# Kernel tuning notes

Measured on AMD Instinct MI355X. Metric: run time of the kernel, lower is better.

The kernel has to match this reference:

```python
import jax, jax.numpy as jnp
import numpy as np

DIM = 48
HEADS = 4
HIDDEN = DIM * 2  # ffn_expansion_factor=2
EPS = 1e-5


def conv3d(x, w, b, groups=1, pad=0):
    # x: [B,C,T,H,W], w: [O, I//groups, kd,kh,kw]
    y = jax.lax.conv_general_dilated(
        x, w, window_strides=(1, 1, 1), padding=[(pad, pad)] * 3,
        dimension_numbers=('NCDHW', 'OIDHW', 'NCDHW'),
        feature_group_count=groups)
    return y + b[None, :, None, None, None]


def layernorm(x, w, b):
    # WithBias LayerNorm over channel dim (dim=1), per spatial position
    mu = jnp.mean(x, axis=1, keepdims=True)
    var = jnp.var(x, axis=1, keepdims=True)
    return (x - mu) / jnp.sqrt(var + EPS) * w[None, :, None, None, None] + b[None, :, None, None, None]


def setup_inputs() -> dict:
    key = jax.random.key(0)
    ks = jax.random.split(key, 16)
    s = 0.02
    inp = {
        'x': jax.random.normal(ks[0], (2, DIM, 16, 64, 64), jnp.float32),
        'ln1_w': jnp.ones((DIM,), jnp.float32),
        'ln1_b': jnp.zeros((DIM,), jnp.float32),
        'qkv_w': jax.random.normal(ks[1], (DIM * 3 * HEADS, DIM, 1, 1, 1), jnp.float32) * s,
        'qkv_b': jnp.zeros((DIM * 3 * HEADS,), jnp.float32),
        'qkvdw_w': jax.random.normal(ks[2], (DIM * 3 * HEADS, HEADS, 3, 3, 3), jnp.float32) * s,
        'qkvdw_b': jnp.zeros((DIM * 3 * HEADS,), jnp.float32),
        'temperature': jnp.ones((HEADS, 1, 1), jnp.float32),
        'proj_w': jax.random.normal(ks[3], (DIM, DIM * HEADS, 1, 1, 1), jnp.float32) * s,
        'proj_b': jnp.zeros((DIM,), jnp.float32),
        'ln2_w': jnp.ones((DIM,), jnp.float32),
        'ln2_b': jnp.zeros((DIM,), jnp.float32),
        'pin_w': jax.random.normal(ks[4], (2 * HIDDEN, DIM, 1, 1, 1), jnp.float32) * s,
        'pin_b': jnp.zeros((2 * HIDDEN,), jnp.float32),
        'dw_w': jax.random.normal(ks[5], (2 * HIDDEN, 1, 3, 3, 3), jnp.float32) * s,
        'dw_b': jnp.zeros((2 * HIDDEN,), jnp.float32),
        'pout_w': jax.random.normal(ks[6], (DIM, HIDDEN, 1, 1, 1), jnp.float32) * s,
        'pout_b': jnp.zeros((DIM,), jnp.float32),
    }
    return inp


def attention(y, qkv_w, qkv_b, qkvdw_w, qkvdw_b, temperature, proj_w, proj_b):
    b, c, t, h, w = y.shape
    n = t * h * w
    qkv = conv3d(y, qkv_w, qkv_b, pad=0)
    qkv = conv3d(qkv, qkvdw_w, qkvdw_b, groups=c * 3, pad=1)  # groups=dim*3
    q, k, v = jnp.split(qkv, 3, axis=1)  # each [b, heads*dim, t,h,w]
    def resh(z):
        return z.reshape(b, HEADS, c, n)  # 'b (head c) t h w -> b head c (thw)'
    q, k, v = resh(q), resh(k), resh(v)
    q = q / jnp.maximum(jnp.linalg.norm(q, axis=-1, keepdims=True), 1e-12)
    k = k / jnp.maximum(jnp.linalg.norm(k, axis=-1, keepdims=True), 1e-12)
    attn = jnp.einsum('bhcn,bhdn->bhcd', q, k) * temperature[None]  # [b,h,c,c]
    attn = jax.nn.softmax(attn, axis=-1)
    out = jnp.einsum('bhcd,bhdn->bhcn', attn, v)
    out = out.reshape(b, HEADS * c, t, h, w)
    return conv3d(out, proj_w, proj_b, pad=0)


def ffn(y, pin_w, pin_b, dw_w, dw_b, pout_w, pout_b):
    z = conv3d(y, pin_w, pin_b, pad=0)
    z = conv3d(z, dw_w, dw_b, groups=2 * HIDDEN, pad=1)
    z1, z2 = jnp.split(z, 2, axis=1)
    z = jax.nn.gelu(z1, approximate=False) * z2
    return conv3d(z, pout_w, pout_b, pad=0)


def reference(x, ln1_w, ln1_b, qkv_w, qkv_b, qkvdw_w, qkvdw_b, temperature,
              proj_w, proj_b, ln2_w, ln2_b, pin_w, pin_b, dw_w, dw_b, pout_w, pout_b):
    x = x + attention(layernorm(x, ln1_w, ln1_b), qkv_w, qkv_b, qkvdw_w, qkvdw_b,
                      temperature, proj_w, proj_b)
    x = x + ffn(layernorm(x, ln2_w, ln2_b), pin_w, pin_b, dw_w, dw_b, pout_w, pout_b)
    return x
```

## Files before the change

kernel.cpp:

```cpp
#include <hip/hip_runtime.h>
#include <hip/hip_bf16.h>
#include <hip/hip_fp16.h>
#include <hip/hip_fp8.h>
#include <math.h>

typedef __hip_bfloat16 bf16;
typedef __attribute__((ext_vector_type(8))) short short8;
typedef __attribute__((ext_vector_type(4))) float f32x4;

#define NPB   65536
#define DIMC  48
#define C2    192
#define HIDC  96
#define TT    16

static __device__ __forceinline__ float b2f(bf16 v) { return __bfloat162float(v); }
static __device__ __forceinline__ bf16  f2b(float v) { return __float2bfloat16(v); }
static __device__ __forceinline__ float bfr2f(unsigned short u) {
  union { unsigned int i; float f; } c; c.i = ((unsigned int)u) << 16; return c.f;
}
static __device__ __forceinline__ unsigned short f2us(float v) {
  return __bfloat16_as_ushort(__float2bfloat16(v));
}
static __device__ __forceinline__ unsigned char f2fp8(float v) {
  __hip_fp8_e4m3 t(v); return (unsigned char)t.__x;
}
static __device__ __forceinline__ float fp82f(unsigned char u) {
  __hip_fp8_e4m3 t; t.__x = (__hip_fp8_storage_t)u; return (float)t;
}

#if defined(__has_builtin)
#if __has_builtin(__builtin_amdgcn_cvt_pk_f32_fp8) && __has_builtin(__builtin_amdgcn_cvt_pk_fp8_f32)
#define HW_FP8 1
#endif
#endif

static __device__ __forceinline__ void fp8x4_to_f32x4(unsigned int u, float* o) {
#ifdef HW_FP8
  auto lo = __builtin_amdgcn_cvt_pk_f32_fp8(u, false);
  auto hi = __builtin_amdgcn_cvt_pk_f32_fp8(u, true);
  o[0] = lo[0]; o[1] = lo[1]; o[2] = hi[0]; o[3] = hi[1];
#else
  o[0] = fp82f(u & 0xff); o[1] = fp82f((u >> 8) & 0xff);
  o[2] = fp82f((u >> 16) & 0xff); o[3] = fp82f((u >> 24) & 0xff);
#endif
}
static __device__ __forceinline__ unsigned int f32x2_to_fp8pair(float x, float y) {
#ifdef HW_FP8
  return (unsigned int)__builtin_amdgcn_cvt_pk_fp8_f32(x, y, 0, false) & 0xffffu;
#else
  return (unsigned int)f2fp8(x) | ((unsigned int)f2fp8(y) << 8);
#endif
}
static __device__ __forceinline__ void fp8pair_to_2f(unsigned int pr, float& x, float& y) {
#ifdef HW_FP8
  auto d = __builtin_amdgcn_cvt_pk_f32_fp8(pr, false);
  x = d[0]; y = d[1];
#else
  x = fp82f(pr & 0xff); y = fp82f((pr >> 8) & 0xff);
#endif
}

static __device__ __forceinline__ unsigned int pkh2(float x, float y) {
  auto h = __builtin_amdgcn_cvt_pkrtz(x, y);
  return __builtin_bit_cast(unsigned int, h);
}
static __device__ __forceinline__ float dot2f16(unsigned int a, unsigned int b, float c) {
  asm("v_dot2_f32_f16 %0, %1, %2, %0" : "+v"(c) : "v"(a), "v"(b));
  return c;
}
static __device__ __forceinline__ __half2 u2h2(unsigned int u) {
  return __builtin_bit_cast(__half2, u);
}

__global__ __launch_bounds__(256) void k_ln(
    const float* __restrict__ x, const float* __restrict__ lw, const float* __restrict__ lb,
    bf16* __restrict__ y) {
  int p = blockIdx.x * 256 + threadIdx.x;
  int b = p >> 16, n = p & (NPB - 1);
  const float* xb = x + ((size_t)b * DIMC) * NPB + n;
  float v[DIMC]; float s = 0.f, s2 = 0.f;
#pragma unroll
  for (int c = 0; c < DIMC; ++c) { float t = xb[(size_t)c * NPB]; v[c] = t; s += t; s2 += t * t; }
  float mu = s * (1.f / DIMC);
  float var = fmaxf(s2 * (1.f / DIMC) - mu * mu, 0.f);
  float rs = rsqrtf(var + 1e-5f);
  bf16* yb = y + ((size_t)b * DIMC) * NPB + n;
#pragma unroll
  for (int c = 0; c < DIMC; ++c) yb[(size_t)c * NPB] = f2b((v[c] - mu) * rs * lw[c] + lb[c]);
}

__global__ __launch_bounds__(256) void k_pconv_sec(
    const bf16* __restrict__ y, const float* __restrict__ W,
    const float* __restrict__ bias, int hp, unsigned char* __restrict__ dst, int dcs) {
  __shared__ unsigned short Yl[64][130];
  __shared__ unsigned short Wl[48][72];
  __shared__ unsigned char Ot[48][132];
  int tid = threadIdx.x;
  int sec = blockIdx.x;
  int row = (hp >= 0) ? ((sec >> 1) * 192 + (2 * hp + (sec & 1)) * 48) : sec * 48;
  int bt = blockIdx.y;
  int b = bt >> 9;
  int n0 = (bt & 511) * 128;
  const unsigned short* yb = (const unsigned short*)(y + ((size_t)b * DIMC) * NPB) + n0;
  for (int j = tid; j < 48 * 32; j += 256) {
    int c = j >> 5, sub = j & 31;
    ushort4 u = *(const ushort4*)(yb + (size_t)c * NPB + sub * 4);
    *(ushort2*)&Yl[c][sub * 4]     = make_ushort2(u.x, u.y);
    *(ushort2*)&Yl[c][sub * 4 + 2] = make_ushort2(u.z, u.w);
  }
  for (int j = tid; j < 16 * 32; j += 256) {
    int c = 48 + (j >> 5), sub = j & 31;
    *(ushort2*)&Yl[c][sub * 4]     = make_ushort2(0, 0);
    *(ushort2*)&Yl[c][sub * 4 + 2] = make_ushort2(0, 0);
  }
  if (tid < 48) {
    const float* wr = W + (size_t)(row + tid) * 48;
    unsigned short* wl = Wl[tid];
#pragma unroll
    for (int c = 0; c < 48; ++c) wl[c] = f2us(wr[c]);
#pragma unroll
    for (int c = 48; c < 64; ++c) wl[c] = 0;
  }
  __syncthreads();
  int wv = tid >> 6, ln = tid & 63, lq = ln >> 4, li = ln & 15;
  short8 afr[3][2];
#pragma unroll
  for (int mt = 0; mt < 3; ++mt)
#pragma unroll
    for (int ks = 0; ks < 2; ++ks)
      afr[mt][ks] = *(const short8*)&Wl[mt * 16 + li][ks * 32 + lq * 8];
#pragma unroll 1
  for (int ns = 0; ns < 2; ++ns) {
    int nn = wv * 32 + ns * 16 + li;
    short8 bfr[2];
#pragma unroll
    for (int ks = 0; ks < 2; ++ks)
#pragma unroll
      for (int j = 0; j < 8; ++j)
        bfr[ks][j] = (short)Yl[ks * 32 + lq * 8 + j][nn];
#pragma unroll
    for (int mt = 0; mt < 3; ++mt) {
      f32x4 acc = {0.f, 0.f, 0.f, 0.f};
      acc = __builtin_amdgcn_mfma_f32_16x16x32_bf16(afr[mt][0], bfr[0], acc, 0, 0, 0);
      acc = __builtin_amdgcn_mfma_f32_16x16x32_bf16(afr[mt][1], bfr[1], acc, 0, 0, 0);
      int m0 = mt * 16 + lq * 4;
      unsigned int p01 = f32x2_to_fp8pair(16.f * (acc[0] + bias[row + m0]),
                                          16.f * (acc[1] + bias[row + m0 + 1]));
      unsigned int p23 = f32x2_to_fp8pair(16.f * (acc[2] + bias[row + m0 + 2]),
                                          16.f * (acc[3] + bias[row + m0 + 3]));
      Ot[m0 + 0][nn] = (unsigned char)p01;
      Ot[m0 + 1][nn] = (unsigned char)(p01 >> 8);
      Ot[m0 + 2][nn] = (unsigned char)p23;
      Ot[m0 + 3][nn] = (unsigned char)(p23 >> 8);
    }
  }
  __syncthreads();
  for (int j = tid; j < 48 * 32; j += 256) {
    int m = j >> 5, c4 = (j & 31) * 4;
    *(uchar4*)(dst + ((size_t)b * dcs + sec * 48 + m) * NPB + n0 + c4) =
        *(const uchar4*)&Ot[m][c4];
  }
}

__global__ __launch_bounds__(512, 8) void k_gconv48(
    const unsigned char* __restrict__ src, int sco,
    const float* __restrict__ gw, const float* __restrict__ gb,
    unsigned char* __restrict__ dst, int hp, int isV, float* __restrict__ sqout) {
  __shared__ unsigned int tile[2][4][18][66];
  __shared__ unsigned int Wh[2][28][4];
  __shared__ float red[8][4];
  int tid = threadIdx.x;
  int t0 = (blockIdx.x >> 2) * 2, h0 = (blockIdx.x & 3) * 16;
  int cbase = blockIdx.y * 4, b = blockIdx.z;
  int seg = cbase / 48, lc = cbase - seg * 48;
  int wbase = isV ? 384 + (2 * hp + seg) * 48 + lc
                  : ((seg >= 2 ? 192 : 0) + (2 * hp + (seg & 1)) * 48 + lc);
  int dch = isV ? (2 * hp + seg) * 48 + lc : cbase;
  const unsigned char* ib = src + ((size_t)b * 288 + sco + cbase) * NPB;
  for (int j = tid; j < 216; j += 512) {
    int o = j & 3, t2 = j >> 2;
    int cp = t2 / 27, tap = t2 - cp * 27;
    const float* wr = gw + (size_t)(wbase + o) * 108 + cp * 54 + tap;
    Wh[cp][tap][o] = pkh2(wr[0], wr[27]);
  }
  for (int j = tid; j < 2304; j += 512) {
    int sub = j & 15, r = j >> 4;
    int cp = r / 72, rem = r - cp * 72;
    int tt = rem / 18, hh = rem - tt * 18;
    int gt = t0 + tt - 1, gh2 = h0 + hh - 1;
    unsigned int* dp = &tile[cp][tt][hh][1 + sub * 4];
    if ((unsigned)gt < 16u && (unsigned)gh2 < 64u) {
      const unsigned char* p0 = ib + (size_t)(2 * cp) * NPB + gt * 4096 + gh2 * 64 + sub * 4;
      unsigned int u0 = *(const unsigned int*)p0;
      unsigned int u1 = *(const unsigned int*)(p0 + NPB);
      float a0[4], a1[4];
      fp8x4_to_f32x4(u0, a0);
      fp8x4_to_f32x4(u1, a1);
      dp[0] = pkh2(a0[0], a1[0]);
      dp[1] = pkh2(a0[1], a1[1]);
      dp[2] = pkh2(a0[2], a1[2]);
      dp[3] = pkh2(a0[3], a1[3]);
    } else { dp[0] = 0; dp[1] = 0; dp[2] = 0; dp[3] = 0; }
  }
  for (int j = tid; j < 288; j += 512) {
    int side = j & 1, r = j >> 1;
    int cp = r / 72, rem = r - cp * 72;
    int tt = rem / 18, hh = rem - tt * 18;
    tile[cp][tt][hh][side ? 65 : 0] = 0;
  }
  __syncthreads();
  int w = tid & 63, hr = tid >> 6;
  float acc[2][2][4];
#pragma unroll
  for (int t = 0; t < 2; ++t)
#pragma unroll
    for (int i = 0; i < 2; ++i)
#pragma unroll
      for (int o = 0; o < 4; ++o) acc[t][i][o] = 0.f;
#pragma unroll 1
  for (int cp = 0; cp < 2; ++cp) {
#pragma unroll 1
    for (int dw = 0; dw < 3; ++dw) {
      int wwl = w + dw;
      unsigned int v[4][4];
#pragma unroll
      for (int tt = 0; tt < 4; ++tt)
#pragma unroll
        for (int r = 0; r < 4; ++r) v[tt][r] = tile[cp][tt][hr * 2 + r][wwl];
#pragma unroll
      for (int dt = 0; dt < 3; ++dt)
#pragma unroll
        for (int dh = 0; dh < 3; ++dh) {
          uint4 wv = *(const uint4*)&Wh[cp][dt * 9 + dh * 3 + dw][0];
#pragma unroll
          for (int t = 0; t < 2; ++t)
#pragma unroll
            for (int i = 0; i < 2; ++i) {
              unsigned int val = v[t + dt][i + dh];
              acc[t][i][0] = dot2f16(val, wv.x, acc[t][i][0]);
              acc[t][i][1] = dot2f16(val, wv.y, acc[t][i][1]);
              acc[t][i][2] = dot2f16(val, wv.z, acc[t][i][2]);
              acc[t][i][3] = dot2f16(val, wv.w, acc[t][i][3]);
            }
        }
    }
  }
  float s[4] = {0.f, 0.f, 0.f, 0.f};
#pragma unroll
  for (int o = 0; o < 4; ++o) {
    float bias16 = 16.f * gb[wbase + o];
    size_t obase = ((size_t)b * 192 + dch + o) * NPB;
#pragma unroll
    for (int t = 0; t < 2; ++t) {
      unsigned int pr = f32x2_to_fp8pair(acc[t][0][o] + bias16, acc[t][1][o] + bias16);
      size_t rb = obase + (t0 + t) * 4096 + (h0 + hr * 2) * 64 + w;
      dst[rb]      = (unsigned char)pr;
      dst[rb + 64] = (unsigned char)(pr >> 8);
      if (sqout) {
        float f0, f1; fp8pair_to_2f(pr, f0, f1);
        s[o] = fmaf(f0, f0, fmaf(f1, f1, s[o]));
      }
    }
  }
  if (sqout) {
#pragma unroll
    for (int o = 0; o < 4; ++o) {
      float sv = s[o];
#pragma unroll
      for (int off = 32; off; off >>= 1) sv += __shfl_down(sv, off);
      if ((tid & 63) == 0) red[tid >> 6][o] = sv;
    }
    __syncthreads();
    if (tid < 4) {
      int sqi = (seg < 2 ? 0 : 384) + b * 192 + (2 * hp + (seg & 1)) * 48 + lc + tid;
      float acc8 = 0.f;
#pragma unroll
      for (int k = 0; k < 8; ++k) acc8 += red[k][tid];
      atomicAdd(&sqout[sqi], acc8);
    }
  }
}

__global__ __launch_bounds__(256) void k_gram_mfma(
    const unsigned char* __restrict__ qkd, int hp, float* __restrict__ Gm) {
  __shared__ unsigned short qkl[2][48][264];
  int tid = threadIdx.x, b = blockIdx.y, z = blockIdx.z;
  int wv = tid >> 6, ln = tid & 63, lq = ln >> 4, li = ln & 15;
  const unsigned char* qb = qkd + ((size_t)b * 192 + z * 48) * NPB + blockIdx.x * 1024;
  const unsigned char* kb = qkd + ((size_t)b * 192 + 96 + z * 48) * NPB + blockIdx.x * 1024;
  f32x4 acc[9];
#pragma unroll
  for (int t = 0; t < 9; ++t) acc[t] = (f32x4){0.f, 0.f, 0.f, 0.f};
#pragma unroll 1
  for (int it = 0; it < 4; ++it) {
    __syncthreads();
    for (int j = tid; j < 48 * 64; j += 256) {
      int c = j >> 6, sub = j & 63;
      unsigned int uq = *(const unsigned int*)(qb + (size_t)c * NPB + it * 256 + sub * 4);
      unsigned int uk = *(const unsigned int*)(kb + (size_t)c * NPB + it * 256 + sub * 4);
      float aq[4], ak[4];
      fp8x4_to_f32x4(uq, aq);
      fp8x4_to_f32x4(uk, ak);
      *(ushort2*)&qkl[0][c][sub * 4]     = make_ushort2(f2us(aq[0]), f2us(aq[1]));
      *(ushort2*)&qkl[0][c][sub * 4 + 2] = make_ushort2(f2us(aq[2]), f2us(aq[3]));
      *(ushort2*)&qkl[1][c][sub * 4]     = make_ushort2(f2us(ak[0]), f2us(ak[1]));
      *(ushort2*)&qkl[1][c][sub * 4 + 2] = make_ushort2(f2us(ak[2]), f2us(ak[3]));
    }
    __syncthreads();
    short8 afr[3][2], bfr[3][2];
#pragma unroll
    for (int ks = 0; ks < 2; ++ks) {
      int kbase = wv * 64 + ks * 32 + lq * 8;
#pragma unroll
      for (int t = 0; t < 3; ++t) {
        afr[t][ks] = *(const short8*)&qkl[0][t * 16 + li][kbase];
        bfr[t][ks] = *(const short8*)&qkl[1][t * 16 + li][kbase];
      }
    }
#pragma unroll
    for (int mt = 0; mt < 3; ++mt)
#pragma unroll
      for (int nt = 0; nt < 3; ++nt) {
        acc[mt * 3 + nt] = __builtin_amdgcn_mfma_f32_16x16x32_bf16(afr[mt][0], bfr[nt][0], acc[mt * 3 + nt], 0, 0, 0);
        acc[mt * 3 + nt] = __builtin_amdgcn_mfma_f32_16x16x32_bf16(afr[mt][1], bfr[nt][1], acc[mt * 3 + nt], 0, 0, 0);
      }
  }
  __syncthreads();
  float* red = (float*)&qkl[0][0][0];
  if (wv > 0) {
    float* rw = red + (size_t)(wv - 1) * 2304;
#pragma unroll
    for (int t = 0; t < 9; ++t)
#pragma unroll
      for (int r = 0; r < 4; ++r)
        rw[t * 256 + r * 64 + ln] = acc[t][r];
  }
  __syncthreads();
  if (wv == 0) {
    int hd = 2 * hp + z;
    float* gbase = Gm + (size_t)(b * 4 + hd) * 2304;
#pragma unroll
    for (int t = 0; t < 9; ++t) {
      int mt = t / 3, nt = t - mt * 3;
#pragma unroll
      for (int r = 0; r < 4; ++r) {
        int o = t * 256 + r * 64 + ln;
        float v = acc[t][r] + red[o] + red[2304 + o] + red[4608 + o];
        atomicAdd(&gbase[(mt * 16 + lq * 4 + r) * 48 + nt * 16 + li], v);
      }
    }
  }
}

__global__ __launch_bounds__(256) void k_attn_mm(
    const float* __restrict__ Gm, const float* __restrict__ sq, const float* __restrict__ temp,
    const float* __restrict__ pw, bf16* __restrict__ Mm) {
  __shared__ float A[48][48];
  __shared__ float nk[48];
  int tid = threadIdx.x;
  int bh = blockIdx.x; int b = bh >> 2, hd = bh & 3;
  if (tid >= 64 && tid < 112)
    nk[tid - 64] = fmaxf(sqrtf(sq[384 + bh * 48 + tid - 64]), 1e-12f);
  __syncthreads();
  if (tid < 48) {
    float tv = temp[hd];
    float rq = 1.f / fmaxf(sqrtf(sq[bh * 48 + tid]), 1e-12f);
    const float* grow = Gm + (size_t)bh * 2304 + tid * 48;
    float mx = -1e30f;
#pragma unroll
    for (int d = 0; d < 48; ++d) mx = fmaxf(mx, grow[d] * rq / nk[d] * tv);
    float sum = 0.f;
#pragma unroll
    for (int d = 0; d < 48; ++d) {
      float e = expf(grow[d] * rq / nk[d] * tv - mx);
      A[tid][d] = e; sum += e;
    }
    float inv = 1.f / sum;
#pragma unroll
    for (int d = 0; d < 48; ++d) A[tid][d] *= inv;
  }
  __syncthreads();
  for (int j = tid; j < 2304; j += 256) {
    int m = j / 48, d = j - m * 48;
    float a = 0.f;
#pragma unroll
    for (int c = 0; c < 48; ++c) a = fmaf(pw[m * 192 + hd * 48 + c], A[c][d], a);
    Mm[((size_t)b * 48 + m) * 192 + hd * 48 + d] = f2b(a * 0.0625f);
  }
}

__global__ __launch_bounds__(256) void k_av192(
    const unsigned char* __restrict__ vd8, const bf16* __restrict__ Mm,
    const float* __restrict__ pb, const float* __restrict__ x, float* __restrict__ outp) {
  __shared__ unsigned short Yl[96][130];
  __shared__ unsigned short Ml[48][200];
  int tid = threadIdx.x;
  int bt = blockIdx.x;
  int b = bt >> 9;
  int n0 = (bt & 511) * 128;
  int wv = tid >> 6, ln = tid & 63, lq = ln >> 4, li = ln & 15;
  const unsigned short* mb = (const unsigned short*)(Mm + (size_t)b * 48 * 192);
  for (int j = tid; j < 48 * 48; j += 256) {
    int m = j / 48, c4 = j - m * 48;
    *(ushort4*)&Ml[m][c4 * 4] = *(const ushort4*)(mb + m * 192 + c4 * 4);
  }
  const unsigned char* vb = vd8 + ((size_t)b * C2) * NPB + n0;
  f32x4 acc[3][2];
#pragma unroll
  for (int mt = 0; mt < 3; ++mt)
#pragma unroll
    for (int ns = 0; ns < 2; ++ns) acc[mt][ns] = (f32x4){0.f, 0.f, 0.f, 0.f};
#pragma unroll 1
  for (int s = 0; s < 2; ++s) {
    __syncthreads();
    for (int j = tid; j < 96 * 32; j += 256) {
      int c = j >> 5, sub = j & 31;
      unsigned int u = *(const unsigned int*)(vb + (size_t)(s * 96 + c) * NPB + sub * 4);
      float a[4]; fp8x4_to_f32x4(u, a);
      *(ushort2*)&Yl[c][sub * 4]     = make_ushort2(f2us(a[0]), f2us(a[1]));
      *(ushort2*)&Yl[c][sub * 4 + 2] = make_ushort2(f2us(a[2]), f2us(a[3]));
    }
    __syncthreads();
#pragma unroll 1
    for (int ns = 0; ns < 2; ++ns) {
      int nn = wv * 32 + ns * 16 + li;
      short8 bfr[3];
#pragma unroll
      for (int ks = 0; ks < 3; ++ks)
#pragma unroll
        for (int j = 0; j < 8; ++j)
          bfr[ks][j] = (short)Yl[ks * 32 + lq * 8 + j][nn];
#pragma unroll
      for (int mt = 0; mt < 3; ++mt) {
        short8 a0 = *(const short8*)&Ml[mt * 16 + li][s * 96 + lq * 8];
        short8 a1 = *(const short8*)&Ml[mt * 16 + li][s * 96 + 32 + lq * 8];
        short8 a2 = *(const short8*)&Ml[mt * 16 + li][s * 96 + 64 + lq * 8];
        acc[mt][ns] = __builtin_amdgcn_mfma_f32_16x16x32_bf16(a0, bfr[0], acc[mt][ns], 0, 0, 0);
        acc[mt][ns] = __builtin_amdgcn_mfma_f32_16x16x32_bf16(a1, bfr[1], acc[mt][ns], 0, 0, 0);
        acc[mt][ns] = __builtin_amdgcn_mfma_f32_16x16x32_bf16(a2, bfr[2], acc[mt][ns], 0, 0, 0);
      }
    }
  }
#pragma unroll
  for (int ns = 0; ns < 2; ++ns) {
    int nn = wv * 32 + ns * 16 + li;
#pragma unroll
    for (int mt = 0; mt < 3; ++mt)
#pragma unroll
      for (int r = 0; r < 4; ++r) {
        int m = mt * 16 + lq * 4 + r;
        size_t idx = ((size_t)b * DIMC + m) * NPB + n0 + nn;
        outp[idx] = x[idx] + pb[m] + acc[mt][ns][r];
      }
  }
}

__global__ __launch_bounds__(256) void k_ek96(
    const unsigned char* __restrict__ V, const float* __restrict__ W, int wrs,
    const float* __restrict__ bias, const float* __restrict__ addend, float* __restrict__ outp) {
  __shared__ unsigned short Yl[96][130];
  __shared__ unsigned short Wl[48][104];
  int tid = threadIdx.x;
  int bt = blockIdx.x;
  int b = bt >> 9;
  int n0 = (bt & 511) * 128;
  const unsigned char* vb = V + ((size_t)b * 96) * NPB + n0;
  for (int j = tid; j < 96 * 32; j += 256) {
    int c = j >> 5, sub = j & 31;
    unsigned int u = *(const unsigned int*)(vb + (size_t)c * NPB + sub * 4);
    float a[4]; fp8x4_to_f32x4(u, a);
    *(ushort2*)&Yl[c][sub * 4]     = make_ushort2(f2us(a[0]), f2us(a[1]));
    *(ushort2*)&Yl[c][sub * 4 + 2] = make_ushort2(f2us(a[2]), f2us(a[3]));
  }
  if (tid < 48) {
    const float* wr = W + (size_t)tid * wrs;
    unsigned short* wl = Wl[tid];
#pragma unroll
    for (int c = 0; c < 96; ++c) wl[c] = f2us(wr[c] * 0.0625f);
  }
  __syncthreads();
  int wv = tid >> 6, ln = tid & 63, lq = ln >> 4, li = ln & 15;
  short8 afr[3][3];
#pragma unroll
  for (int mt = 0; mt < 3; ++mt)
#pragma unroll
    for (int ks = 0; ks < 3; ++ks)
      afr[mt][ks] = *(const short8*)&Wl[mt * 16 + li][ks * 32 + lq * 8];
#pragma unroll 1
  for (int ns = 0; ns < 2; ++ns) {
    int nn = wv * 32 + ns * 16 + li;
    short8 bfr[3];
#pragma unroll
    for (int ks = 0; ks < 3; ++ks)
#pragma unroll
      for (int j = 0; j < 8; ++j)
        bfr[ks][j] = (short)Yl[ks * 32 + lq * 8 + j][nn];
#pragma unroll
    for (int mt = 0; mt < 3; ++mt) {
      f32x4 acc = {0.f, 0.f, 0.f, 0.f};
      acc = __builtin_amdgcn_mfma_f32_16x16x32_bf16(afr[mt][0], bfr[0], acc, 0, 0, 0);
      acc = __builtin_amdgcn_mfma_f32_16x16x32_bf16(afr[mt][1], bfr[1], acc, 0, 0, 0);
      acc = __builtin_amdgcn_mfma_f32_16x16x32_bf16(afr[mt][2], bfr[2], acc, 0, 0, 0);
#pragma unroll
      for (int r = 0; r < 4; ++r) {
        int m = mt * 16 + lq * 4 + r;
        size_t idx = ((size_t)b * DIMC + m) * NPB + n0 + nn;
        outp[idx] = acc[r] + addend[idx] + bias[m];
      }
    }
  }
}

__global__ __launch_bounds__(256) void k_dw_gelu(
    const unsigned char* __restrict__ z, const float* __restrict__ dwW,
    const float* __restrict__ dwB, unsigned char* __restrict__ g) {
  __shared__ unsigned int tile[4][18][68];
  int tid = threadIdx.x;
  int t0 = (blockIdx.x >> 2) * 2, h0 = (blockIdx.x & 3) * 16;
  int c = blockIdx.y, b = blockIdx.z;
  int wq = tid & 15, hq = tid >> 4;
  int w0 = wq * 4;
  const unsigned char* zp0 = z + ((size_t)b * C2 + c) * NPB;
  const unsigned char* zp1 = zp0 + (size_t)HIDC * NPB;
  for (int j = tid; j < 72 * 16; j += 256) {
    int r = j >> 4, sub = j & 15;
    int tt = r / 18, hh = r - tt * 18;
    int gt = t0 + tt - 1, gh = h0 + hh - 1;
    unsigned int* dp = &tile[tt][hh][1 + sub * 4];
    if ((unsigned)gt < 16u && (unsigned)gh < 64u) {
      size_t off = (size_t)gt * 4096 + gh * 64 + sub * 4;
      unsigned int u0 = *(const unsigned int*)(zp0 + off);
      unsigned int u1 = *(const unsigned int*)(zp1 + off);
      float a0[4], a1[4];
      fp8x4_to_f32x4(u0, a0);
      fp8x4_to_f32x4(u1, a1);
      dp[0] = pkh2(a0[0], a1[0]);
      dp[1] = pkh2(a0[1], a1[1]);
      dp[2] = pkh2(a0[2], a1[2]);
      dp[3] = pkh2(a0[3], a1[3]);
    } else { dp[0] = 0; dp[1] = 0; dp[2] = 0; dp[3] = 0; }
  }
  for (int j = tid; j < 144; j += 256) {
    int r = j >> 1, side = j & 1;
    int tt = r / 18, hh = r - tt * 18;
    tile[tt][hh][side ? 65 : 0] = 0;
  }
  unsigned int wpk[27];
  {
    const float* wt0 = dwW + (size_t)c * 27;
    const float* wt1 = dwW + (size_t)(c + HIDC) * 27;
#pragma unroll
    for (int tap = 0; tap < 27; ++tap) wpk[tap] = pkh2(wt0[tap], wt1[tap]);
  }
  __syncthreads();
  __half2 hacc[2][4];
#pragma unroll
  for (int t = 0; t < 2; ++t)
#pragma unroll
    for (int k = 0; k < 4; ++k) hacc[t][k] = u2h2(0u);
#pragma unroll 1
  for (int dh = 0; dh < 3; ++dh) {
    unsigned int v[4][6];
#pragma unroll
    for (int tt = 0; tt < 4; ++tt) {
      uint4 q4 = *(const uint4*)&tile[tt][hq + dh][w0];
      uint2 q2 = *(const uint2*)&tile[tt][hq + dh][w0 + 4];
      v[tt][0] = q4.x; v[tt][1] = q4.y; v[tt][2] = q4.z; v[tt][3] = q4.w;
      v[tt][4] = q2.x; v[tt][5] = q2.y;
    }
#pragma unroll
    for (int dt = 0; dt < 3; ++dt)
#pragma unroll
      for (int dw = 0; dw < 3; ++dw) {
        __half2 wk = u2h2(wpk[dt * 9 + dh * 3 + dw]);
#pragma unroll
        for (int t = 0; t < 2; ++t)
#pragma unroll
          for (int k = 0; k < 4; ++k)
            hacc[t][k] = __hfma2(u2h2(v[t + dt][dw + k]), wk, hacc[t][k]);
      }
  }
  float b1 = dwB[c], b2v = dwB[c + HIDC];
  size_t obase = ((size_t)b * HIDC + c) * NPB;
#pragma unroll
  for (int t = 0; t < 2; ++t) {
    float e[4];
#pragma unroll
    for (int k = 0; k < 4; ++k) {
      float x1v = __low2float(hacc[t][k]) * 0.0625f + b1;
      float x2v = __high2float(hacc[t][k]) * 0.0625f + b2v;
      float ge = 0.5f * x1v * (1.f + erff(x1v * 0.70710678118654752f));
      e[k] = 16.f * ge * x2v;
    }
    unsigned int p01 = f32x2_to_fp8pair(e[0], e[1]);
    unsigned int p23 = f32x2_to_fp8pair(e[2], e[3]);
    unsigned int packed = p01 | (p23 << 16);
    *(unsigned int*)(g + obase + (t0 + t) * 4096 + (h0 + hq) * 64 + w0) = packed;
  }
}

extern "C" void kernel_launch(void* const* d_in, const int* in_sizes, int n_in,
                              void* d_out, int out_size, void* d_ws, size_t ws_size,
                              hipStream_t stream) {
  (void)in_sizes; (void)n_in; (void)out_size; (void)ws_size;
  const float* x     = (const float*)d_in[0];
  const float* ln1w  = (const float*)d_in[1];
  const float* ln1b  = (const float*)d_in[2];
  const float* qkvw  = (const float*)d_in[3];
  const float* qkvb  = (const float*)d_in[4];
  const float* gdww  = (const float*)d_in[5];
  const float* gdwb  = (const float*)d_in[6];
  const float* temp  = (const float*)d_in[7];
  const float* projw = (const float*)d_in[8];
  const float* projb = (const float*)d_in[9];
  const float* ln2w  = (const float*)d_in[10];
  const float* ln2b  = (const float*)d_in[11];
  const float* pinw  = (const float*)d_in[12];
  const float* pinb  = (const float*)d_in[13];
  const float* dww   = (const float*)d_in[14];
  const float* dwb   = (const float*)d_in[15];
  const float* poutw = (const float*)d_in[16];
  const float* poutb = (const float*)d_in[17];
  float* out = (float*)d_out;

  char* ws = (char*)d_ws;
  bf16*  y     = (bf16*)(ws);
  unsigned char* st288 = (unsigned char*)(ws + 12582912);
  unsigned char* vd8   = (unsigned char*)(ws + 50331648);
  float* Gm    = (float*)(ws + 75497472);
  float* sq    = (float*)(ws + 75571200);
  bf16*  Mm    = (bf16*)(ws + 75574272);
  unsigned char* qkd8 = (unsigned char*)d_out;
  bf16*  y2    = (bf16*)(ws);
  unsigned char* z8  = (unsigned char*)(ws + 12582912);
  unsigned char* gg8 = (unsigned char*)(ws + 37748736);

  (void)hipMemsetAsync(Gm, 0, 73728 + 3072, stream);
  k_ln<<<dim3(512), dim3(256), 0, stream>>>(x, ln1w, ln1b, y);

  for (int hp = 0; hp < 2; ++hp) {
    k_pconv_sec<<<dim3(6, 1024), dim3(256), 0, stream>>>(y, qkvw, qkvb, hp, st288, 288);
    k_gconv48<<<dim3(32, 48, 2), dim3(512), 0, stream>>>(
        st288, 0, gdww, gdwb, qkd8, hp, 0, sq);
    k_gram_mfma<<<dim3(64, 2, 2), dim3(256), 0, stream>>>(qkd8, hp, Gm);
    k_gconv48<<<dim3(32, 24, 2), dim3(512), 0, stream>>>(
        st288, 192, gdww, gdwb, vd8, hp, 1, nullptr);
  }
  k_attn_mm<<<dim3(8), dim3(256), 0, stream>>>(Gm, sq, temp, projw, Mm);
  k_av192<<<dim3(1024), dim3(256), 0, stream>>>(vd8, Mm, projb, x, out);

  k_ln<<<dim3(512), dim3(256), 0, stream>>>(out, ln2w, ln2b, y2);
  k_pconv_sec<<<dim3(4, 1024), dim3(256), 0, stream>>>(y2, pinw, pinb, -1, z8, 192);
  k_dw_gelu<<<dim3(32, 96, 2), dim3(256), 0, stream>>>(z8, dww, dwb, gg8);
  k_ek96<<<dim3(1024), dim3(256), 0, stream>>>(gg8, poutw, 96, poutb, out, out);
}
```

Before: 522.9 us.

## Rewrite grouped 3x3x3 conv as MFMA with block-diagonal weights

```diff
diff --git a/kernel.cpp b/kernel.cpp
--- a/kernel.cpp
+++ b/kernel.cpp
@@ -72,6 +72,7 @@
 static __device__ __forceinline__ __half2 u2h2(unsigned int u) {
   return __builtin_bit_cast(__half2, u);
 }
+static __device__ __forceinline__ int swz8(int c) { return c ^ ((c >> 4) & 7); }
 
 __global__ __launch_bounds__(256) void k_ln(
     const float* __restrict__ x, const float* __restrict__ lw, const float* __restrict__ lb,
@@ -163,121 +164,129 @@
   }
 }
 
-__global__ __launch_bounds__(512, 8) void k_gconv48(
+__global__ __launch_bounds__(512, 4) void k_gconv48(
     const unsigned char* __restrict__ src, int sco,
     const float* __restrict__ gw, const float* __restrict__ gb,
     unsigned char* __restrict__ dst, int hp, int isV, float* __restrict__ sqout) {
-  __shared__ unsigned int tile[2][4][18][66];
-  __shared__ unsigned int Wh[2][28][4];
-  __shared__ float red[8][4];
+  __shared__ unsigned char lds[42240];
   int tid = threadIdx.x;
-  int t0 = (blockIdx.x >> 2) * 2, h0 = (blockIdx.x & 3) * 16;
-  int cbase = blockIdx.y * 4, b = blockIdx.z;
-  int seg = cbase / 48, lc = cbase - seg * 48;
+  int t0 = (blockIdx.x >> 3) * 2, h0 = (blockIdx.x & 7) * 8;
+  int cb = blockIdx.y * 16, b = blockIdx.z;
+  int seg = cb / 48, lc = cb - seg * 48;
   int wbase = isV ? 384 + (2 * hp + seg) * 48 + lc
                   : ((seg >= 2 ? 192 : 0) + (2 * hp + (seg & 1)) * 48 + lc);
-  int dch = isV ? (2 * hp + seg) * 48 + lc : cbase;
-  const unsigned char* ib = src + ((size_t)b * 288 + sco + cbase) * NPB;
-  for (int j = tid; j < 216; j += 512) {
-    int o = j & 3, t2 = j >> 2;
-    int cp = t2 / 27, tap = t2 - cp * 27;
-    const float* wr = gw + (size_t)(wbase + o) * 108 + cp * 54 + tap;
-    Wh[cp][tap][o] = pkh2(wr[0], wr[27]);
-  }
-  for (int j = tid; j < 2304; j += 512) {
-    int sub = j & 15, r = j >> 4;
-    int cp = r / 72, rem = r - cp * 72;
-    int tt = rem / 18, hh = rem - tt * 18;
-    int gt = t0 + tt - 1, gh2 = h0 + hh - 1;
-    unsigned int* dp = &tile[cp][tt][hh][1 + sub * 4];
-    if ((unsigned)gt < 16u && (unsigned)gh2 < 64u) {
-      const unsigned char* p0 = ib + (size_t)(2 * cp) * NPB + gt * 4096 + gh2 * 64 + sub * 4;
-      unsigned int u0 = *(const unsigned int*)p0;
-      unsigned int u1 = *(const unsigned int*)(p0 + NPB);
-      float a0[4], a1[4];
-      fp8x4_to_f32x4(u0, a0);
-      fp8x4_to_f32x4(u1, a1);
-      dp[0] = pkh2(a0[0], a1[0]);
-      dp[1] = pkh2(a0[1], a1[1]);
-      dp[2] = pkh2(a0[2], a1[2]);
-      dp[3] = pkh2(a0[3], a1[3]);
-    } else { dp[0] = 0; dp[1] = 0; dp[2] = 0; dp[3] = 0; }
-  }
-  for (int j = tid; j < 288; j += 512) {
-    int side = j & 1, r = j >> 1;
-    int cp = r / 72, rem = r - cp * 72;
-    int tt = rem / 18, hh = rem - tt * 18;
-    tile[cp][tt][hh][side ? 65 : 0] = 0;
-  }
-  __syncthreads();
-  int w = tid & 63, hr = tid >> 6;
-  float acc[2][2][4];
-#pragma unroll
-  for (int t = 0; t < 2; ++t)
-#pragma unroll
-    for (int i = 0; i < 2; ++i)
-#pragma unroll
-      for (int o = 0; o < 4; ++o) acc[t][i][o] = 0.f;
-#pragma unroll 1
-  for (int cp = 0; cp < 2; ++cp) {
-#pragma unroll 1
-    for (int dw = 0; dw < 3; ++dw) {
-      int wwl = w + dw;
-      unsigned int v[4][4];
-#pragma unroll
-      for (int tt = 0; tt < 4; ++tt)
-#pragma unroll
-        for (int r = 0; r < 4; ++r) v[tt][r] = tile[cp][tt][hr * 2 + r][wwl];
-#pragma unroll
-      for (int dt = 0; dt < 3; ++dt)
-#pragma unroll
-        for (int dh = 0; dh < 3; ++dh) {
-          uint4 wv = *(const uint4*)&Wh[cp][dt * 9 + dh * 3 + dw][0];
-#pragma unroll
-          for (int t = 0; t < 2; ++t)
-#pragma unroll
-            for (int i = 0; i < 2; ++i) {
-              unsigned int val = v[t + dt][i + dh];
-              acc[t][i][0] = dot2f16(val, wv.x, acc[t][i][0]);
-              acc[t][i][1] = dot2f16(val, wv.y, acc[t][i][1]);
-              acc[t][i][2] = dot2f16(val, wv.z, acc[t][i][2]);
-              acc[t][i][3] = dot2f16(val, wv.w, acc[t][i][3]);
-            }
-        }
-    }
-  }
-  float s[4] = {0.f, 0.f, 0.f, 0.f};
-#pragma unroll
-  for (int o = 0; o < 4; ++o) {
-    float bias16 = 16.f * gb[wbase + o];
-    size_t obase = ((size_t)b * 192 + dch + o) * NPB;
-#pragma unroll
-    for (int t = 0; t < 2; ++t) {
-      unsigned int pr = f32x2_to_fp8pair(acc[t][0][o] + bias16, acc[t][1][o] + bias16);
-      size_t rb = obase + (t0 + t) * 4096 + (h0 + hr * 2) * 64 + w;
-      dst[rb]      = (unsigned char)pr;
-      dst[rb + 64] = (unsigned char)(pr >> 8);
-      if (sqout) {
-        float f0, f1; fp8pair_to_2f(pr, f0, f1);
-        s[o] = fmaf(f0, f0, fmaf(f1, f1, s[o]));
-      }
+  int dch = isV ? (2 * hp + seg) * 48 + lc : cb;
+  const unsigned char* ib = src + ((size_t)b * 288 + sco + cb) * NPB;
+
+#pragma unroll 1
+  for (int ch = 0; ch < 16; ++ch) {
+    const unsigned char* chp = ib + (size_t)ch * NPB;
+    int hi = ch >> 3, lo = ch & 7;
+    for (int j = tid; j < 640; j += 512) {
+      int tt = j / 160, rem = j - tt * 160, hh = rem >> 4, sub = rem & 15;
+      int gt = t0 + tt - 1, gh = h0 + hh - 1;
+      uchar4 u = make_uchar4(0, 0, 0, 0);
+      if ((unsigned)gt < 16u && (unsigned)gh < 64u)
+        u = *(const uchar4*)(chp + (size_t)gt * 4096 + gh * 64 + sub * 4);
+      int cell = (tt * 10 + hh) * 66 + 1 + sub * 4;
+      lds[swz8((cell + 0) * 2 + hi) * 8 + lo] = u.x;
+      lds[swz8((cell + 1) * 2 + hi) * 8 + lo] = u.y;
+      lds[swz8((cell + 2) * 2 + hi) * 8 + lo] = u.z;
+      lds[swz8((cell + 3) * 2 + hi) * 8 + lo] = u.w;
+    }
+  }
+  for (int j = tid; j < 160; j += 512) {
+    int half = j & 1, side = (j >> 1) & 1, r = j >> 2;
+    int tt = r / 10, hh = r - tt * 10;
+    int cell = (tt * 10 + hh) * 66 + (side ? 65 : 0);
+    *(unsigned long long*)&lds[swz8(cell * 2 + half) * 8] = 0ull;
+  }
+
+  int ln = tid & 63, li = ln & 15, lq = ln >> 4;
+  int g4 = (li >> 2) * 4;
+  int chb = (lq & 1) * 8;
+  int lqh = lq >> 1;
+  const float* wrow = gw + (size_t)(wbase + li) * 108;
+  short8 bw[14];
+#pragma unroll
+  for (int p = 0; p < 14; ++p) {
+    int tap = 2 * p + lqh;
+    union { unsigned int u[4]; short8 s; } cv;
+#pragma unroll
+    for (int jj = 0; jj < 4; ++jj) {
+      int ch0 = chb + jj * 2, ch1 = ch0 + 1;
+      float f0 = (tap < 27 && ch0 >= g4 && ch0 < g4 + 4) ? wrow[(ch0 - g4) * 27 + tap] : 0.f;
+      float f1 = (tap < 27 && ch1 >= g4 && ch1 < g4 + 4) ? wrow[(ch1 - g4) * 27 + tap] : 0.f;
+      cv.u[jj] = pkh2(f0, f1);
+    }
+    bw[p] = cv.s;
+  }
+  __syncthreads();
+
+  int wvv = tid >> 6;
+  unsigned int outp[8];
+  float bias16 = 16.f * gb[wbase + li];
+#pragma unroll 1
+  for (int tl = 0; tl < 8; ++tl) {
+    int tile_id = wvv * 8 + tl;
+    int t_o = tile_id >> 5, h_o = (tile_id >> 2) & 7, w0 = (tile_id & 3) << 4;
+    int cbase = (t_o * 10 + h_o) * 66 + w0 + li;
+    f32x4 acc = {0.f, 0.f, 0.f, 0.f};
+#pragma unroll
+    for (int p = 0; p < 14; ++p) {
+      int tA = 2 * p, tB = 2 * p + 1;
+      int offA = ((tA / 9) * 10 + (tA % 9) / 3) * 66 + tA % 3;
+      int offB = (tB < 27) ? (((tB / 9) * 10 + (tB % 9) / 3) * 66 + tB % 3) : 0;
+      int off = (lqh ? offB : offA);
+      short8 af;
+      if (2 * p + lqh < 27) {
+        int c = (cbase + off) * 2 + (lq & 1);
+        uint2 raw = *(const uint2*)&lds[swz8(c) * 8];
+        float f[8];
+        fp8x4_to_f32x4(raw.x, f);
+        fp8x4_to_f32x4(raw.y, f + 4);
+        union { unsigned int u[4]; short8 s; } cv;
+        cv.u[0] = pkh2(f[0], f[1]); cv.u[1] = pkh2(f[2], f[3]);
+        cv.u[2] = pkh2(f[4], f[5]); cv.u[3] = pkh2(f[6], f[7]);
+        af = cv.s;
+      } else {
+        af = (short8){0, 0, 0, 0, 0, 0, 0, 0};
+      }
+      acc = __builtin_amdgcn_mfma_f32_16x16x32_f16(af, bw[p], acc, 0, 0, 0);
+    }
+    unsigned int p01 = f32x2_to_fp8pair(acc[0] + bias16, acc[1] + bias16);
+    unsigned int p23 = f32x2_to_fp8pair(acc[2] + bias16, acc[3] + bias16);
+    outp[tl] = (p01 & 0xffffu) | (p23 << 16);
+  }
+  __syncthreads();
+#pragma unroll
+  for (int tl = 0; tl < 8; ++tl) {
+    int tile_id = wvv * 8 + tl;
+    int t_o = tile_id >> 5, h_o = (tile_id >> 2) & 7, w0 = (tile_id & 3) << 4;
+    int pos = t_o * 512 + h_o * 64 + w0 + lq * 4;
+    *(unsigned int*)&lds[li * 1040 + pos] = outp[tl];
+  }
+  __syncthreads();
+  int oc = tid >> 5, lp = tid & 31;
+  size_t obase = ((size_t)b * 192 + dch + oc) * NPB;
+  float s = 0.f;
+#pragma unroll
+  for (int k2 = 0; k2 < 8; ++k2) {
+    int pos = (lp + k2 * 32) * 4;
+    unsigned int v = *(const unsigned int*)&lds[oc * 1040 + pos];
+    int t = pos >> 9, h = (pos >> 6) & 7, w = pos & 63;
+    *(unsigned int*)(dst + obase + (size_t)(t0 + t) * 4096 + (h0 + h) * 64 + w) = v;
+    if (sqout) {
+      float f[4]; fp8x4_to_f32x4(v, f);
+      s += f[0] * f[0] + f[1] * f[1] + f[2] * f[2] + f[3] * f[3];
     }
   }
   if (sqout) {
 #pragma unroll
-    for (int o = 0; o < 4; ++o) {
-      float sv = s[o];
-#pragma unroll
-      for (int off = 32; off; off >>= 1) sv += __shfl_down(sv, off);
-      if ((tid & 63) == 0) red[tid >> 6][o] = sv;
-    }
-    __syncthreads();
-    if (tid < 4) {
-      int sqi = (seg < 2 ? 0 : 384) + b * 192 + (2 * hp + (seg & 1)) * 48 + lc + tid;
-      float acc8 = 0.f;
-#pragma unroll
-      for (int k = 0; k < 8; ++k) acc8 += red[k][tid];
-      atomicAdd(&sqout[sqi], acc8);
+    for (int off = 16; off; off >>= 1) s += __shfl_down(s, off, 32);
+    if (lp == 0) {
+      int sqi = (seg < 2 ? 0 : 384) + b * 192 + (2 * hp + (seg & 1)) * 48 + lc + oc;
+      atomicAdd(&sqout[sqi], s);
     }
   }
 }
@@ -641,10 +650,10 @@
 
   for (int hp = 0; hp < 2; ++hp) {
     k_pconv_sec<<<dim3(6, 1024), dim3(256), 0, stream>>>(y, qkvw, qkvb, hp, st288, 288);
-    k_gconv48<<<dim3(32, 48, 2), dim3(512), 0, stream>>>(
+    k_gconv48<<<dim3(64, 12, 2), dim3(512), 0, stream>>>(
         st288, 0, gdww, gdwb, qkd8, hp, 0, sq);
     k_gram_mfma<<<dim3(64, 2, 2), dim3(256), 0, stream>>>(qkd8, hp, Gm);
-    k_gconv48<<<dim3(32, 24, 2), dim3(512), 0, stream>>>(
+    k_gconv48<<<dim3(64, 6, 2), dim3(512), 0, stream>>>(
         st288, 192, gdww, gdwb, vd8, hp, 1, nullptr);
   }
   k_attn_mm<<<dim3(8), dim3(256), 0, stream>>>(Gm, sq, temp, projw, Mm);
```

Measured after the change: 669.0 us. +27.9%, slower.
